# Kernel optimization log

Measured on AMD Instinct MI355X. Metric: run time of the kernel, lower is better.

## Reference

```python
import jax, jax.numpy as jnp
import numpy as np

B, S, D, DOUT = 16, 1024, 768, 256
TEMP = D ** 0.5


def setup_inputs() -> dict:
    key = jax.random.key(0)
    ks = jax.random.split(key, 16)
    emb = jax.random.normal(ks[0], (B, S, D), dtype=jnp.float32)
    mask = jax.random.randint(ks[1], (B, S), 0, 2, dtype=jnp.int32)
    scale = 0.02
    def lin(kw, kb, din, dout):
        return (jax.random.normal(kw, (din, dout), dtype=jnp.float32) * scale,
                jax.random.normal(kb, (dout,), dtype=jnp.float32) * scale)
    q_Wq, q_bq = lin(ks[2], ks[3], D, D)
    q_Wk, q_bk = lin(ks[4], ks[5], D, D)
    q_Wv, q_bv = lin(ks[6], ks[7], D, DOUT)
    d_Wq, d_bq = lin(ks[8], ks[9], D, D)
    d_Wk, d_bk = lin(ks[10], ks[11], D, D)
    d_Wv, d_bv = lin(ks[12], ks[13], D, DOUT)
    return {
        'emb': emb, 'mask': mask, 'is_query': 1,
        'query_Wq': q_Wq, 'query_bq': q_bq,
        'query_Wk': q_Wk, 'query_bk': q_bk,
        'query_Wv': q_Wv, 'query_bv': q_bv,
        'doc_Wq': d_Wq, 'doc_bq': d_bq,
        'doc_Wk': d_Wk, 'doc_bk': d_bk,
        'doc_Wv': d_Wv, 'doc_bv': d_bv,
    }


def reference(emb, mask, is_query,
              query_Wq, query_bq, query_Wk, query_bk, query_Wv, query_bv,
              doc_Wq, doc_bq, doc_Wk, doc_bk, doc_Wv, doc_bv):
    # is_query is a static Python int/bool selecting the projection set
    if is_query:
        Wq, bq, Wk, bk, Wv, bv = query_Wq, query_bq, query_Wk, query_bk, query_Wv, query_bv
    else:
        Wq, bq, Wk, bk, Wv, bv = doc_Wq, doc_bq, doc_Wk, doc_bk, doc_Wv, doc_bv
    q = jnp.einsum('bsd,de->bse', emb, Wq) + bq  # [B,S,D]
    k = jnp.einsum('bsd,de->bse', emb, Wk) + bk  # [B,S,D]
    v = jnp.einsum('bsd,de->bse', emb, Wv) + bv  # [B,S,DOUT]
    attn = jnp.einsum('bqd,bkd->bqk', q / TEMP, k)  # [B,S,S]
    attn = jnp.where(mask[:, None, :] == 0, jnp.float32(-1e9), attn)
    attn = jax.nn.softmax(attn, axis=-1)
    out = jnp.einsum('bqk,bkd->bqd', attn, v)  # [B,S,DOUT]
    return out, attn
```

## Files before the change

kernel.cpp:

```cpp
#include <hip/hip_runtime.h>
#include <hip/hip_bf16.h>

static constexpr float INV_TEMP = 0.03608439182435161f;

typedef __attribute__((ext_vector_type(8))) short bf16x8;
typedef __attribute__((ext_vector_type(4))) float f32x4;
typedef __attribute__((ext_vector_type(8))) unsigned short u16x8;
typedef __attribute__((ext_vector_type(4))) unsigned short u16x4;

__device__ __forceinline__ unsigned short f2bf(float f) {
  unsigned u = __float_as_uint(f);
  u += 0x7fffu + ((u >> 16) & 1u);
  return (unsigned short)(u >> 16);
}

__device__ __forceinline__ void async_copy16(const void* g, void* lds) {
  __builtin_amdgcn_global_load_lds(
      (const __attribute__((address_space(1))) unsigned int*)g,
      (__attribute__((address_space(3))) unsigned int*)lds, 16, 0, 0);
}

__global__ __launch_bounds__(256) void pack_emb(const float* __restrict__ src,
                                                unsigned short* __restrict__ dst) {
  long i = ((long)blockIdx.x * 256 + threadIdx.x) * 8;
  float4 a = *(const float4*)(src + i);
  float4 b = *(const float4*)(src + i + 4);
  u16x8 v;
  v[0] = f2bf(a.x); v[1] = f2bf(a.y); v[2] = f2bf(a.z); v[3] = f2bf(a.w);
  v[4] = f2bf(b.x); v[5] = f2bf(b.y); v[6] = f2bf(b.z); v[7] = f2bf(b.w);
  *(u16x8*)(dst + i) = v;
}

__global__ __launch_bounds__(256) void pack_w(
    const int* __restrict__ isq_p,
    const float* qWq, const float* qbq, const float* qWk, const float* qbk,
    const float* qWv, const float* qbv,
    const float* dWq, const float* dbq, const float* dWk, const float* dbk,
    const float* dWv, const float* dbv,
    unsigned short* __restrict__ WT, float* __restrict__ bias) {
  const int n = blockIdx.x;
  const int isq = *isq_p;
  const float* W; const float* bsrc; int col, srcN;
  if (n < 768)       { W = isq ? qWq : dWq; bsrc = isq ? qbq : dbq; col = n;        srcN = 768; }
  else if (n < 1536) { W = isq ? qWk : dWk; bsrc = isq ? qbk : dbk; col = n - 768;  srcN = 768; }
  else               { W = isq ? qWv : dWv; bsrc = isq ? qbv : dbv; col = n - 1536; srcN = 256; }
#pragma unroll
  for (int i = 0; i < 3; ++i) {
    int d = threadIdx.x + i * 256;
    WT[(long)n * 768 + d] = f2bf(W[(long)d * srcN + col]);
  }
  if (threadIdx.x == 0) bias[n] = bsrc[col];
}

template <int MODE>
__global__ __launch_bounds__(512, 2) void gemm256(
    const unsigned short* __restrict__ A, long lda, long strideA,
    const unsigned short* __restrict__ BT, long ldb, long strideB,
    void* __restrict__ Cv, long ldc, long strideC,
    const float* __restrict__ bias, float scale, int K) {
  extern __shared__ unsigned short smem[];
  const int tid = threadIdx.x;
  const int wid = tid >> 6, lane = tid & 63;
  const int wr = wid >> 2, wc = wid & 3;
  const int fr = lane & 15, fq = lane >> 4;
  const int bz = blockIdx.z;
  const unsigned short* Apan = A + (long)bz * strideA + (long)blockIdx.x * 256 * lda;
  const unsigned short* Bpan = BT + (long)bz * strideB + (long)blockIdx.y * 256 * ldb;
  const int nk = K >> 6;

  auto stage = [&](int tile, int mat, int ks, int buf) {
    const unsigned short* g = (mat ? Bpan : Apan) + (long)tile * 64 + ks * 32;
    const long ld = mat ? ldb : lda;
    unsigned short* d = smem + (((buf << 2) | (mat << 1) | ks) << 13);
#pragma unroll
    for (int i = 0; i < 2; ++i) {
      const int e = (tid + i * 512) * 8;
      const int row = e >> 5;
      const int sl = (e >> 3) & 3;
      const int ss = sl ^ ((row >> 1) & 3);
      async_copy16(g + (long)row * ld + ss * 8, d + e);
    }
  };

  const int fro = fr * 32 + ((fq ^ ((fr >> 1) & 3)) << 3);
  const int awo = fro + (wr * 128) * 32;
  const int bwo = fro + (wc * 64) * 32;

  bf16x8 a[8];
  f32x4 acc[8][4];
#pragma unroll
  for (int m = 0; m < 8; ++m)
#pragma unroll
    for (int n = 0; n < 4; ++n) acc[m][n] = f32x4{0.f, 0.f, 0.f, 0.f};

  stage(0, 0, 0, 0); stage(0, 1, 0, 0); stage(0, 0, 1, 0); stage(0, 1, 1, 0);
  if (nk > 1) {
    stage(1, 0, 0, 1); stage(1, 1, 0, 1); stage(1, 0, 1, 1);
    asm volatile("s_waitcnt vmcnt(6)" ::: "memory");
  } else {
    asm volatile("s_waitcnt vmcnt(0)" ::: "memory");
  }
  __builtin_amdgcn_sched_barrier(0);
  __builtin_amdgcn_s_barrier();

  for (int t = 0; t < nk; ++t) {
    const int p = t & 1;
    const unsigned short* A0 = smem + (((p << 2) | 0) << 13);
    const unsigned short* A1 = smem + (((p << 2) | 1) << 13);
    const unsigned short* B0 = smem + (((p << 2) | 2) << 13);
    const unsigned short* B1 = smem + (((p << 2) | 3) << 13);

    {
#pragma unroll
      for (int m = 0; m < 8; ++m) a[m] = *(const bf16x8*)(A0 + awo + m * 512);
      bf16x8 b0 = *(const bf16x8*)(B0 + bwo + 0 * 512);
      bf16x8 b1 = *(const bf16x8*)(B0 + bwo + 1 * 512);
      if (t + 1 < nk) stage(t + 1, 1, 1, (t + 1) & 1);
      __builtin_amdgcn_s_barrier();
      asm volatile("s_waitcnt lgkmcnt(0)");
      __builtin_amdgcn_sched_barrier(0);
      __builtin_amdgcn_s_setprio(1);
#pragma unroll
      for (int m = 0; m < 8; ++m) {
        acc[m][0] = __builtin_amdgcn_mfma_f32_16x16x32_bf16(a[m], b0, acc[m][0], 0, 0, 0);
        acc[m][1] = __builtin_amdgcn_mfma_f32_16x16x32_bf16(a[m], b1, acc[m][1], 0, 0, 0);
      }
      __builtin_amdgcn_s_setprio(0);
      __builtin_amdgcn_sched_barrier(0);
      __builtin_amdgcn_s_barrier();
    }
    {
      bf16x8 b2 = *(const bf16x8*)(B0 + bwo + 2 * 512);
      bf16x8 b3 = *(const bf16x8*)(B0 + bwo + 3 * 512);
      if (t + 2 < nk) stage(t + 2, 0, 0, p);
      __builtin_amdgcn_s_barrier();
      asm volatile("s_waitcnt lgkmcnt(0)");
      __builtin_amdgcn_sched_barrier(0);
      __builtin_amdgcn_s_setprio(1);
#pragma unroll
      for (int m = 0; m < 8; ++m) {
        acc[m][2] = __builtin_amdgcn_mfma_f32_16x16x32_bf16(a[m], b2, acc[m][2], 0, 0, 0);
        acc[m][3] = __builtin_amdgcn_mfma_f32_16x16x32_bf16(a[m], b3, acc[m][3], 0, 0, 0);
      }
      __builtin_amdgcn_s_setprio(0);
      __builtin_amdgcn_sched_barrier(0);
      __builtin_amdgcn_s_barrier();
    }
    {
#pragma unroll
      for (int m = 0; m < 8; ++m) a[m] = *(const bf16x8*)(A1 + awo + m * 512);
      bf16x8 b0 = *(const bf16x8*)(B1 + bwo + 0 * 512);
      bf16x8 b1 = *(const bf16x8*)(B1 + bwo + 1 * 512);
      if (t + 2 < nk) stage(t + 2, 1, 0, p);
      __builtin_amdgcn_s_barrier();
      asm volatile("s_waitcnt lgkmcnt(0)");
      __builtin_amdgcn_sched_barrier(0);
      __builtin_amdgcn_s_setprio(1);
#pragma unroll
      for (int m = 0; m < 8; ++m) {
        acc[m][0] = __builtin_amdgcn_mfma_f32_16x16x32_bf16(a[m], b0, acc[m][0], 0, 0, 0);
        acc[m][1] = __builtin_amdgcn_mfma_f32_16x16x32_bf16(a[m], b1, acc[m][1], 0, 0, 0);
      }
      __builtin_amdgcn_s_setprio(0);
      __builtin_amdgcn_sched_barrier(0);
      __builtin_amdgcn_s_barrier();
    }
    {
      bf16x8 b2 = *(const bf16x8*)(B1 + bwo + 2 * 512);
      bf16x8 b3 = *(const bf16x8*)(B1 + bwo + 3 * 512);
      if (t + 2 < nk) stage(t + 2, 0, 1, p);
      __builtin_amdgcn_s_barrier();
      asm volatile("s_waitcnt lgkmcnt(0)");
      __builtin_amdgcn_sched_barrier(0);
      __builtin_amdgcn_s_setprio(1);
#pragma unroll
      for (int m = 0; m < 8; ++m) {
        acc[m][2] = __builtin_amdgcn_mfma_f32_16x16x32_bf16(a[m], b2, acc[m][2], 0, 0, 0);
        acc[m][3] = __builtin_amdgcn_mfma_f32_16x16x32_bf16(a[m], b3, acc[m][3], 0, 0, 0);
      }
      __builtin_amdgcn_s_setprio(0);
      if (t < nk - 2) {
        asm volatile("s_waitcnt vmcnt(6)" ::: "memory");
      } else if (t == nk - 2) {
        asm volatile("s_waitcnt vmcnt(0)" ::: "memory");
      }
      __builtin_amdgcn_sched_barrier(0);
      __builtin_amdgcn_s_barrier();
    }
  }

  const long m0 = (long)blockIdx.x * 256 + wr * 128;
  const long n0 = (long)blockIdx.y * 256 + wc * 64;
#pragma unroll
  for (int m = 0; m < 8; ++m) {
#pragma unroll
    for (int n = 0; n < 4; ++n) {
      const long mm = m0 + m * 16 + fq * 4;
      const long nn = n0 + n * 16 + fr;
      f32x4 v = acc[m][n];
      if (MODE == 0) {
        unsigned short* C = (unsigned short*)Cv + (long)bz * strideC;
        const float bb = bias[nn];
#pragma unroll
        for (int r = 0; r < 4; ++r) C[(mm + r) * ldc + nn] = f2bf(v[r] + bb);
      } else {
        float* C = (float*)Cv + (long)bz * strideC;
#pragma unroll
        for (int r = 0; r < 4; ++r) C[(mm + r) * ldc + nn] = v[r] * scale;
      }
    }
  }
}

template <int MODE>
__global__ __launch_bounds__(256) void gemm_bt(
    const unsigned short* __restrict__ A, long lda, long strideA,
    const unsigned short* __restrict__ BT, long ldb, long strideB,
    void* __restrict__ Cv, long ldc, long strideC,
    const float* __restrict__ bias, float scale, int K) {
  __shared__ unsigned short Ab[2][128 * 32];
  __shared__ unsigned short Bb[2][128 * 32];
  const int tid = threadIdx.x, wid = tid >> 6, lane = tid & 63;
  const int bz = blockIdx.z;
  A  += (long)bz * strideA + (long)blockIdx.x * 128 * lda;
  BT += (long)bz * strideB + (long)blockIdx.y * 128 * ldb;
  const int srow = lane >> 2;
  const int skk  = (lane & 3) * 8;

  auto stage = [&](int buf, int kt) {
    const unsigned short* As = A + (long)kt * 32;
    const unsigned short* Bs = BT + (long)kt * 32;
#pragma unroll
    for (int i = 0; i < 2; ++i) {
      int c = wid * 2 + i;
      async_copy16(As + (long)(c * 16 + srow) * lda + skk, &Ab[buf][c * 512]);
      async_copy16(Bs + (long)(c * 16 + srow) * ldb + skk, &Bb[buf][c * 512]);
    }
  };

  f32x4 acc[4][4] = {};
  const int nk = K / 32;
  stage(0, 0);
  __syncthreads();
  int buf = 0;
  const int wr = wid >> 1, wc = wid & 1;
  const int fr = lane & 15, fq = lane >> 4;
  for (int kt = 0; kt < nk; ++kt) {
    if (kt + 1 < nk) stage(buf ^ 1, kt + 1);
    const unsigned short* Ap = &Ab[buf][(wr * 64 + fr) * 32 + fq * 8];
    const unsigned short* Bp = &Bb[buf][(wc * 64 + fr) * 32 + fq * 8];
    bf16x8 af[4], bfv[4];
#pragma unroll
    for (int mi = 0; mi < 4; ++mi) af[mi] = *(const bf16x8*)(Ap + mi * 16 * 32);
#pragma unroll
    for (int ni = 0; ni < 4; ++ni) bfv[ni] = *(const bf16x8*)(Bp + ni * 16 * 32);
#pragma unroll
    for (int mi = 0; mi < 4; ++mi)
#pragma unroll
      for (int ni = 0; ni < 4; ++ni)
        acc[mi][ni] = __builtin_amdgcn_mfma_f32_16x16x32_bf16(af[mi], bfv[ni], acc[mi][ni], 0, 0, 0);
    __syncthreads();
    buf ^= 1;
  }

  const long m0 = (long)blockIdx.x * 128 + wr * 64;
  const long n0 = (long)blockIdx.y * 128 + wc * 64;
#pragma unroll
  for (int mi = 0; mi < 4; ++mi) {
#pragma unroll
    for (int ni = 0; ni < 4; ++ni) {
      const long m = m0 + mi * 16 + fq * 4;
      const long n = n0 + ni * 16 + fr;
      f32x4 v = acc[mi][ni];
      if (MODE == 1) {
        unsigned short* C = (unsigned short*)Cv + (long)bz * strideC;
#pragma unroll
        for (int r = 0; r < 4; ++r) C[(m + r) * ldc + n] = f2bf(v[r] + bias[m + r]);
      } else {
        float* C = (float*)Cv + (long)bz * strideC;
#pragma unroll
        for (int r = 0; r < 4; ++r) C[(m + r) * ldc + n] = v[r] * scale;
      }
    }
  }
}

__global__ __launch_bounds__(256) void softmax_rows(float* __restrict__ attn,
                                                    const int* __restrict__ mask,
                                                    unsigned short* __restrict__ attn_bf) {
  const int row = blockIdx.x;
  const int b = row >> 10;
  float* p = attn + (long)row * 1024;
  const int tid = threadIdx.x, lane = tid & 63, wid = tid >> 6;
  float4 v = ((const float4*)p)[tid];
  int4 mk = ((const int4*)(mask + b * 1024))[tid];
  v.x = mk.x ? v.x : -1e9f;
  v.y = mk.y ? v.y : -1e9f;
  v.z = mk.z ? v.z : -1e9f;
  v.w = mk.w ? v.w : -1e9f;
  float mx = fmaxf(fmaxf(v.x, v.y), fmaxf(v.z, v.w));
#pragma unroll
  for (int off = 32; off; off >>= 1) mx = fmaxf(mx, __shfl_xor(mx, off));
  __shared__ float red[4];
  if (lane == 0) red[wid] = mx;
  __syncthreads();
  mx = fmaxf(fmaxf(red[0], red[1]), fmaxf(red[2], red[3]));
  float e0 = __expf(v.x - mx), e1 = __expf(v.y - mx);
  float e2 = __expf(v.z - mx), e3 = __expf(v.w - mx);
  float s = e0 + e1 + e2 + e3;
#pragma unroll
  for (int off = 32; off; off >>= 1) s += __shfl_xor(s, off);
  __shared__ float red2[4];
  if (lane == 0) red2[wid] = s;
  __syncthreads();
  s = red2[0] + red2[1] + red2[2] + red2[3];
  const float inv = 1.0f / s;
  float4 o;
  o.x = e0 * inv; o.y = e1 * inv; o.z = e2 * inv; o.w = e3 * inv;
  ((float4*)p)[tid] = o;
  u16x4 ob;
  ob[0] = f2bf(o.x); ob[1] = f2bf(o.y); ob[2] = f2bf(o.z); ob[3] = f2bf(o.w);
  *(u16x4*)(attn_bf + (long)row * 1024 + tid * 4) = ob;
}

extern "C" void kernel_launch(void* const* d_in, const int* in_sizes, int n_in,
                              void* d_out, int out_size, void* d_ws, size_t ws_size,
                              hipStream_t stream) {
  const float* emb = (const float*)d_in[0];
  const int* mask = (const int*)d_in[1];
  const int* isq = (const int*)d_in[2];
  const float* qWq = (const float*)d_in[3];  const float* qbq = (const float*)d_in[4];
  const float* qWk = (const float*)d_in[5];  const float* qbk = (const float*)d_in[6];
  const float* qWv = (const float*)d_in[7];  const float* qbv = (const float*)d_in[8];
  const float* dWq = (const float*)d_in[9];  const float* dbq = (const float*)d_in[10];
  const float* dWk = (const float*)d_in[11]; const float* dbk = (const float*)d_in[12];
  const float* dWv = (const float*)d_in[13]; const float* dbv = (const float*)d_in[14];

  char* ws = (char*)d_ws;
  unsigned short* emb_bf = (unsigned short*)ws;  ws += (size_t)16384 * 768 * 2;
  unsigned short* WT     = (unsigned short*)ws;  ws += (size_t)1792 * 768 * 2;
  float*          bias   = (float*)ws;           ws += (size_t)1792 * 4;
  unsigned short* QK     = (unsigned short*)ws;  ws += (size_t)16384 * 1536 * 2;
  unsigned short* VT     = (unsigned short*)ws;  ws += (size_t)256 * 16384 * 2;
  unsigned short* attnbf = (unsigned short*)ws;  ws += (size_t)16 * 1024 * 1024 * 2;

  float* out = (float*)d_out;
  float* attn = out + (size_t)16 * 1024 * 256;

  (void)hipFuncSetAttribute((const void*)&gemm256<0>,
                            hipFuncAttributeMaxDynamicSharedMemorySize, 131072);
  (void)hipFuncSetAttribute((const void*)&gemm256<2>,
                            hipFuncAttributeMaxDynamicSharedMemorySize, 131072);

  hipLaunchKernelGGL(pack_emb, dim3(6144), dim3(256), 0, stream, emb, emb_bf);
  hipLaunchKernelGGL(pack_w, dim3(1792), dim3(256), 0, stream, isq,
                     qWq, qbq, qWk, qbk, qWv, qbv, dWq, dbq, dWk, dbk, dWv, dbv, WT, bias);
  hipLaunchKernelGGL((gemm256<0>), dim3(64, 6, 1), dim3(512), 131072, stream,
                     emb_bf, 768L, 0L, WT, 768L, 0L, (void*)QK, 1536L, 0L, bias, 1.0f, 768);
  hipLaunchKernelGGL((gemm_bt<1>), dim3(2, 128, 1), dim3(256), 0, stream,
                     WT + (size_t)1536 * 768, 768L, 0L, emb_bf, 768L, 0L,
                     (void*)VT, 16384L, 0L, bias + 1536, 1.0f, 768);
  hipLaunchKernelGGL((gemm256<2>), dim3(4, 4, 16), dim3(512), 131072, stream,
                     QK, 1536L, (long)1024 * 1536, QK + 768, 1536L, (long)1024 * 1536,
                     (void*)attn, 1024L, (long)1024 * 1024, nullptr, INV_TEMP, 768);
  hipLaunchKernelGGL(softmax_rows, dim3(16384), dim3(256), 0, stream, attn, mask, attnbf);
  hipLaunchKernelGGL((gemm_bt<2>), dim3(8, 2, 16), dim3(256), 0, stream,
                     attnbf, 1024L, (long)1024 * 1024, VT, 16384L, 1024L,
                     (void*)out, 256L, (long)1024 * 256, nullptr, 1.0f, 1024);
}
```

Measured before the change: 183.3 us.

## Merge QK and V projections into one launch, restage k-loop, retile PV GEMM

Merges the QK projection GEMM and the transposed V projection GEMM into a single 448-block launch that shares a common 256x256 k-loop. This removes one launch and lets the small V GEMM run alongside the big one. The k-loop now splits its four quarter-phases along M (4x4 MFMA blocks) instead of along N, and the prefetch order and vmcnt waits change to match. The PV GEMM is retiled from 128x128 to 128x64 output tiles, doubling its grid to 512 blocks for better occupancy at the cost of more reloads of the A operand.

```diff
diff --git a/kernel.cpp b/kernel.cpp
--- a/kernel.cpp
+++ b/kernel.cpp
@@ -52,21 +52,14 @@
   if (threadIdx.x == 0) bias[n] = bsrc[col];
 }
 
-template <int MODE>
-__global__ __launch_bounds__(512, 2) void gemm256(
-    const unsigned short* __restrict__ A, long lda, long strideA,
-    const unsigned short* __restrict__ BT, long ldb, long strideB,
-    void* __restrict__ Cv, long ldc, long strideC,
-    const float* __restrict__ bias, float scale, int K) {
-  extern __shared__ unsigned short smem[];
+__device__ __forceinline__ void k_loop_256(
+    const unsigned short* __restrict__ Apan, long lda,
+    const unsigned short* __restrict__ Bpan, long ldb,
+    int nk, unsigned short* smem, f32x4 (&acc)[8][4]) {
   const int tid = threadIdx.x;
   const int wid = tid >> 6, lane = tid & 63;
   const int wr = wid >> 2, wc = wid & 3;
   const int fr = lane & 15, fq = lane >> 4;
-  const int bz = blockIdx.z;
-  const unsigned short* Apan = A + (long)bz * strideA + (long)blockIdx.x * 256 * lda;
-  const unsigned short* Bpan = BT + (long)bz * strideB + (long)blockIdx.y * 256 * ldb;
-  const int nk = K >> 6;
 
   auto stage = [&](int tile, int mat, int ks, int buf) {
     const unsigned short* g = (mat ? Bpan : Apan) + (long)tile * 64 + ks * 32;
@@ -86,17 +79,10 @@
   const int awo = fro + (wr * 128) * 32;
   const int bwo = fro + (wc * 64) * 32;
 
-  bf16x8 a[8];
-  f32x4 acc[8][4];
-#pragma unroll
-  for (int m = 0; m < 8; ++m)
-#pragma unroll
-    for (int n = 0; n < 4; ++n) acc[m][n] = f32x4{0.f, 0.f, 0.f, 0.f};
-
   stage(0, 0, 0, 0); stage(0, 1, 0, 0); stage(0, 0, 1, 0); stage(0, 1, 1, 0);
   if (nk > 1) {
-    stage(1, 0, 0, 1); stage(1, 1, 0, 1); stage(1, 0, 1, 1);
-    asm volatile("s_waitcnt vmcnt(6)" ::: "memory");
+    stage(1, 0, 0, 1); stage(1, 1, 1, 1);
+    asm volatile("s_waitcnt vmcnt(4)" ::: "memory");
   } else {
     asm volatile("s_waitcnt vmcnt(0)" ::: "memory");
   }
@@ -109,123 +95,182 @@
     const unsigned short* A1 = smem + (((p << 2) | 1) << 13);
     const unsigned short* B0 = smem + (((p << 2) | 2) << 13);
     const unsigned short* B1 = smem + (((p << 2) | 3) << 13);
-
-    {
-#pragma unroll
-      for (int m = 0; m < 8; ++m) a[m] = *(const bf16x8*)(A0 + awo + m * 512);
-      bf16x8 b0 = *(const bf16x8*)(B0 + bwo + 0 * 512);
-      bf16x8 b1 = *(const bf16x8*)(B0 + bwo + 1 * 512);
-      if (t + 1 < nk) stage(t + 1, 1, 1, (t + 1) & 1);
-      __builtin_amdgcn_s_barrier();
-      asm volatile("s_waitcnt lgkmcnt(0)");
-      __builtin_amdgcn_sched_barrier(0);
-      __builtin_amdgcn_s_setprio(1);
-#pragma unroll
-      for (int m = 0; m < 8; ++m) {
-        acc[m][0] = __builtin_amdgcn_mfma_f32_16x16x32_bf16(a[m], b0, acc[m][0], 0, 0, 0);
-        acc[m][1] = __builtin_amdgcn_mfma_f32_16x16x32_bf16(a[m], b1, acc[m][1], 0, 0, 0);
+    bf16x8 a[4], b[4];
+
+#pragma unroll
+    for (int m = 0; m < 4; ++m) a[m] = *(const bf16x8*)(A0 + awo + m * 512);
+#pragma unroll
+    for (int n = 0; n < 4; ++n) b[n] = *(const bf16x8*)(B0 + bwo + n * 512);
+    if (t + 1 < nk) stage(t + 1, 0, 1, (t + 1) & 1);
+    __builtin_amdgcn_s_barrier();
+    asm volatile("s_waitcnt lgkmcnt(0)");
+    __builtin_amdgcn_sched_barrier(0);
+    __builtin_amdgcn_s_setprio(1);
+#pragma unroll
+    for (int m = 0; m < 4; ++m)
+#pragma unroll
+      for (int n = 0; n < 4; ++n)
+        acc[m][n] = __builtin_amdgcn_mfma_f32_16x16x32_bf16(a[m], b[n], acc[m][n], 0, 0, 0);
+    __builtin_amdgcn_s_setprio(0);
+    __builtin_amdgcn_sched_barrier(0);
+    __builtin_amdgcn_s_barrier();
+
+#pragma unroll
+    for (int m = 0; m < 4; ++m) a[m] = *(const bf16x8*)(A0 + awo + (4 + m) * 512);
+    if (t + 1 < nk) stage(t + 1, 1, 0, (t + 1) & 1);
+    __builtin_amdgcn_s_barrier();
+    asm volatile("s_waitcnt lgkmcnt(0)");
+    __builtin_amdgcn_sched_barrier(0);
+    __builtin_amdgcn_s_setprio(1);
+#pragma unroll
+    for (int m = 0; m < 4; ++m)
+#pragma unroll
+      for (int n = 0; n < 4; ++n)
+        acc[4 + m][n] = __builtin_amdgcn_mfma_f32_16x16x32_bf16(a[m], b[n], acc[4 + m][n], 0, 0, 0);
+    __builtin_amdgcn_s_setprio(0);
+    __builtin_amdgcn_sched_barrier(0);
+    __builtin_amdgcn_s_barrier();
+
+#pragma unroll
+    for (int m = 0; m < 4; ++m) a[m] = *(const bf16x8*)(A1 + awo + m * 512);
+#pragma unroll
+    for (int n = 0; n < 4; ++n) b[n] = *(const bf16x8*)(B1 + bwo + n * 512);
+    if (t + 2 < nk) stage(t + 2, 0, 0, p);
+    __builtin_amdgcn_s_barrier();
+    asm volatile("s_waitcnt lgkmcnt(0)");
+    __builtin_amdgcn_sched_barrier(0);
+    __builtin_amdgcn_s_setprio(1);
+#pragma unroll
+    for (int m = 0; m < 4; ++m)
+#pragma unroll
+      for (int n = 0; n < 4; ++n)
+        acc[m][n] = __builtin_amdgcn_mfma_f32_16x16x32_bf16(a[m], b[n], acc[m][n], 0, 0, 0);
+    __builtin_amdgcn_s_setprio(0);
+    __builtin_amdgcn_sched_barrier(0);
+    __builtin_amdgcn_s_barrier();
+
+#pragma unroll
+    for (int m = 0; m < 4; ++m) a[m] = *(const bf16x8*)(A1 + awo + (4 + m) * 512);
+    if (t + 2 < nk) stage(t + 2, 1, 1, p);
+    __builtin_amdgcn_s_barrier();
+    asm volatile("s_waitcnt lgkmcnt(0)");
+    __builtin_amdgcn_sched_barrier(0);
+    __builtin_amdgcn_s_setprio(1);
+#pragma unroll
+    for (int m = 0; m < 4; ++m)
+#pragma unroll
+      for (int n = 0; n < 4; ++n)
+        acc[4 + m][n] = __builtin_amdgcn_mfma_f32_16x16x32_bf16(a[m], b[n], acc[4 + m][n], 0, 0, 0);
+    __builtin_amdgcn_s_setprio(0);
+    if (t < nk - 2) {
+      asm volatile("s_waitcnt vmcnt(4)" ::: "memory");
+    } else if (t == nk - 2) {
+      asm volatile("s_waitcnt vmcnt(0)" ::: "memory");
+    }
+    __builtin_amdgcn_sched_barrier(0);
+    __builtin_amdgcn_s_barrier();
+  }
+}
+
+__global__ __launch_bounds__(512, 2) void proj256(
+    const unsigned short* __restrict__ emb_bf,
+    const unsigned short* __restrict__ WT,
+    const float* __restrict__ bias,
+    unsigned short* __restrict__ QK,
+    unsigned short* __restrict__ VT) {
+  extern __shared__ unsigned short smem[];
+  const int id = blockIdx.x;
+  const unsigned short* Apan;
+  const unsigned short* Bpan;
+  if (id < 384) {
+    Apan = emb_bf + (long)(id & 63) * 256 * 768;
+    Bpan = WT + (long)(id >> 6) * 256 * 768;
+  } else {
+    Apan = WT + (long)1536 * 768;
+    Bpan = emb_bf + (long)(id - 384) * 256 * 768;
+  }
+  f32x4 acc[8][4];
+#pragma unroll
+  for (int m = 0; m < 8; ++m)
+#pragma unroll
+    for (int n = 0; n < 4; ++n) acc[m][n] = f32x4{0.f, 0.f, 0.f, 0.f};
+
+  k_loop_256(Apan, 768, Bpan, 768, 12, smem, acc);
+
+  const int wid = threadIdx.x >> 6, lane = threadIdx.x & 63;
+  const int wr = wid >> 2, wc = wid & 3;
+  const int fr = lane & 15, fq = lane >> 4;
+  if (id < 384) {
+    const long x = id & 63, y = id >> 6;
+#pragma unroll
+    for (int m = 0; m < 8; ++m)
+#pragma unroll
+      for (int n = 0; n < 4; ++n) {
+        const long mm = x * 256 + wr * 128 + m * 16 + fq * 4;
+        const long nn = y * 256 + wc * 64 + n * 16 + fr;
+        const float bb = bias[nn];
+        f32x4 v = acc[m][n];
+#pragma unroll
+        for (int r = 0; r < 4; ++r) QK[(mm + r) * 1536 + nn] = f2bf(v[r] + bb);
       }
-      __builtin_amdgcn_s_setprio(0);
-      __builtin_amdgcn_sched_barrier(0);
-      __builtin_amdgcn_s_barrier();
+  } else {
+    const long v0 = id - 384;
+#pragma unroll
+    for (int m = 0; m < 8; ++m)
+#pragma unroll
+      for (int n = 0; n < 4; ++n) {
+        const long mm = wr * 128 + m * 16 + fq * 4;
+        const long nn = v0 * 256 + wc * 64 + n * 16 + fr;
+        f32x4 v = acc[m][n];
+#pragma unroll
+        for (int r = 0; r < 4; ++r)
+          VT[(mm + r) * 16384 + nn] = f2bf(v[r] + bias[1536 + mm + r]);
+      }
+  }
+}
+
+__global__ __launch_bounds__(512, 2) void logits256(
+    const unsigned short* __restrict__ QK, float* __restrict__ attn) {
+  extern __shared__ unsigned short smem[];
+  const int bz = blockIdx.z;
+  const unsigned short* Apan = QK + (long)bz * 1024 * 1536 + (long)blockIdx.x * 256 * 1536;
+  const unsigned short* Bpan = QK + 768 + (long)bz * 1024 * 1536 + (long)blockIdx.y * 256 * 1536;
+  f32x4 acc[8][4];
+#pragma unroll
+  for (int m = 0; m < 8; ++m)
+#pragma unroll
+    for (int n = 0; n < 4; ++n) acc[m][n] = f32x4{0.f, 0.f, 0.f, 0.f};
+
+  k_loop_256(Apan, 1536, Bpan, 1536, 12, smem, acc);
+
+  const int wid = threadIdx.x >> 6, lane = threadIdx.x & 63;
+  const int wr = wid >> 2, wc = wid & 3;
+  const int fr = lane & 15, fq = lane >> 4;
+  float* C = attn + (long)bz * 1024 * 1024;
+#pragma unroll
+  for (int m = 0; m < 8; ++m)
+#pragma unroll
+    for (int n = 0; n < 4; ++n) {
+      const long mm = (long)blockIdx.x * 256 + wr * 128 + m * 16 + fq * 4;
+      const long nn = (long)blockIdx.y * 256 + wc * 64 + n * 16 + fr;
+      f32x4 v = acc[m][n];
+#pragma unroll
+      for (int r = 0; r < 4; ++r) C[(mm + r) * 1024 + nn] = v[r] * INV_TEMP;
     }
-    {
-      bf16x8 b2 = *(const bf16x8*)(B0 + bwo + 2 * 512);
-      bf16x8 b3 = *(const bf16x8*)(B0 + bwo + 3 * 512);
-      if (t + 2 < nk) stage(t + 2, 0, 0, p);
-      __builtin_amdgcn_s_barrier();
-      asm volatile("s_waitcnt lgkmcnt(0)");
-      __builtin_amdgcn_sched_barrier(0);
-      __builtin_amdgcn_s_setprio(1);
-#pragma unroll
-      for (int m = 0; m < 8; ++m) {
-        acc[m][2] = __builtin_amdgcn_mfma_f32_16x16x32_bf16(a[m], b2, acc[m][2], 0, 0, 0);
-        acc[m][3] = __builtin_amdgcn_mfma_f32_16x16x32_bf16(a[m], b3, acc[m][3], 0, 0, 0);
-      }
-      __builtin_amdgcn_s_setprio(0);
-      __builtin_amdgcn_sched_barrier(0);
-      __builtin_amdgcn_s_barrier();
-    }
-    {
-#pragma unroll
-      for (int m = 0; m < 8; ++m) a[m] = *(const bf16x8*)(A1 + awo + m * 512);
-      bf16x8 b0 = *(const bf16x8*)(B1 + bwo + 0 * 512);
-      bf16x8 b1 = *(const bf16x8*)(B1 + bwo + 1 * 512);
-      if (t + 2 < nk) stage(t + 2, 1, 0, p);
-      __builtin_amdgcn_s_barrier();
-      asm volatile("s_waitcnt lgkmcnt(0)");
-      __builtin_amdgcn_sched_barrier(0);
-      __builtin_amdgcn_s_setprio(1);
-#pragma unroll
-      for (int m = 0; m < 8; ++m) {
-        acc[m][0] = __builtin_amdgcn_mfma_f32_16x16x32_bf16(a[m], b0, acc[m][0], 0, 0, 0);
-        acc[m][1] = __builtin_amdgcn_mfma_f32_16x16x32_bf16(a[m], b1, acc[m][1], 0, 0, 0);
-      }
-      __builtin_amdgcn_s_setprio(0);
-      __builtin_amdgcn_sched_barrier(0);
-      __builtin_amdgcn_s_barrier();
-    }
-    {
-      bf16x8 b2 = *(const bf16x8*)(B1 + bwo + 2 * 512);
-      bf16x8 b3 = *(const bf16x8*)(B1 + bwo + 3 * 512);
-      if (t + 2 < nk) stage(t + 2, 0, 1, p);
-      __builtin_amdgcn_s_barrier();
-      asm volatile("s_waitcnt lgkmcnt(0)");
-      __builtin_amdgcn_sched_barrier(0);
-      __builtin_amdgcn_s_setprio(1);
-#pragma unroll
-      for (int m = 0; m < 8; ++m) {
-        acc[m][2] = __builtin_amdgcn_mfma_f32_16x16x32_bf16(a[m], b2, acc[m][2], 0, 0, 0);
-        acc[m][3] = __builtin_amdgcn_mfma_f32_16x16x32_bf16(a[m], b3, acc[m][3], 0, 0, 0);
-      }
-      __builtin_amdgcn_s_setprio(0);
-      if (t < nk - 2) {
-        asm volatile("s_waitcnt vmcnt(6)" ::: "memory");
-      } else if (t == nk - 2) {
-        asm volatile("s_waitcnt vmcnt(0)" ::: "memory");
-      }
-      __builtin_amdgcn_sched_barrier(0);
-      __builtin_amdgcn_s_barrier();
-    }
-  }
-
-  const long m0 = (long)blockIdx.x * 256 + wr * 128;
-  const long n0 = (long)blockIdx.y * 256 + wc * 64;
-#pragma unroll
-  for (int m = 0; m < 8; ++m) {
-#pragma unroll
-    for (int n = 0; n < 4; ++n) {
-      const long mm = m0 + m * 16 + fq * 4;
-      const long nn = n0 + n * 16 + fr;
-      f32x4 v = acc[m][n];
-      if (MODE == 0) {
-        unsigned short* C = (unsigned short*)Cv + (long)bz * strideC;
-        const float bb = bias[nn];
-#pragma unroll
-        for (int r = 0; r < 4; ++r) C[(mm + r) * ldc + nn] = f2bf(v[r] + bb);
-      } else {
-        float* C = (float*)Cv + (long)bz * strideC;
-#pragma unroll
-        for (int r = 0; r < 4; ++r) C[(mm + r) * ldc + nn] = v[r] * scale;
-      }
-    }
-  }
-}
-
-template <int MODE>
-__global__ __launch_bounds__(256) void gemm_bt(
-    const unsigned short* __restrict__ A, long lda, long strideA,
-    const unsigned short* __restrict__ BT, long ldb, long strideB,
-    void* __restrict__ Cv, long ldc, long strideC,
-    const float* __restrict__ bias, float scale, int K) {
+}
+
+__global__ __launch_bounds__(256) void gemm_pv(
+    const unsigned short* __restrict__ attnbf,
+    const unsigned short* __restrict__ VT,
+    float* __restrict__ out) {
   __shared__ unsigned short Ab[2][128 * 32];
-  __shared__ unsigned short Bb[2][128 * 32];
+  __shared__ unsigned short Bb[2][64 * 32];
   const int tid = threadIdx.x, wid = tid >> 6, lane = tid & 63;
   const int bz = blockIdx.z;
-  A  += (long)bz * strideA + (long)blockIdx.x * 128 * lda;
-  BT += (long)bz * strideB + (long)blockIdx.y * 128 * ldb;
+  const unsigned short* A = attnbf + (long)bz * 1024 * 1024 + (long)blockIdx.x * 128 * 1024;
+  const unsigned short* BT = VT + (long)bz * 1024 + (long)blockIdx.y * 64 * 16384;
   const int srow = lane >> 2;
-  const int skk  = (lane & 3) * 8;
+  const int skk = (lane & 3) * 8;
 
   auto stage = [&](int buf, int kt) {
     const unsigned short* As = A + (long)kt * 32;
@@ -233,13 +278,13 @@
 #pragma unroll
     for (int i = 0; i < 2; ++i) {
       int c = wid * 2 + i;
-      async_copy16(As + (long)(c * 16 + srow) * lda + skk, &Ab[buf][c * 512]);
-      async_copy16(Bs + (long)(c * 16 + srow) * ldb + skk, &Bb[buf][c * 512]);
+      async_copy16(As + (long)(c * 16 + srow) * 1024 + skk, &Ab[buf][c * 512]);
     }
+    async_copy16(Bs + (long)(wid * 16 + srow) * 16384 + skk, &Bb[buf][wid * 512]);
   };
 
-  f32x4 acc[4][4] = {};
-  const int nk = K / 32;
+  f32x4 acc[4][2] = {};
+  const int nk = 32;
   stage(0, 0);
   __syncthreads();
   int buf = 0;
@@ -248,41 +293,34 @@
   for (int kt = 0; kt < nk; ++kt) {
     if (kt + 1 < nk) stage(buf ^ 1, kt + 1);
     const unsigned short* Ap = &Ab[buf][(wr * 64 + fr) * 32 + fq * 8];
-    const unsigned short* Bp = &Bb[buf][(wc * 64 + fr) * 32 + fq * 8];
-    bf16x8 af[4], bfv[4];
+    const unsigned short* Bp = &Bb[buf][(wc * 32 + fr) * 32 + fq * 8];
+    bf16x8 af[4], bfv[2];
 #pragma unroll
     for (int mi = 0; mi < 4; ++mi) af[mi] = *(const bf16x8*)(Ap + mi * 16 * 32);
 #pragma unroll
-    for (int ni = 0; ni < 4; ++ni) bfv[ni] = *(const bf16x8*)(Bp + ni * 16 * 32);
+    for (int ni = 0; ni < 2; ++ni) bfv[ni] = *(const bf16x8*)(Bp + ni * 16 * 32);
 #pragma unroll
     for (int mi = 0; mi < 4; ++mi)
 #pragma unroll
-      for (int ni = 0; ni < 4; ++ni)
+      for (int ni = 0; ni < 2; ++ni)
         acc[mi][ni] = __builtin_amdgcn_mfma_f32_16x16x32_bf16(af[mi], bfv[ni], acc[mi][ni], 0, 0, 0);
     __syncthreads();
     buf ^= 1;
   }
 
+  float* C = out + (long)bz * 1024 * 256;
   const long m0 = (long)blockIdx.x * 128 + wr * 64;
-  const long n0 = (long)blockIdx.y * 128 + wc * 64;
-#pragma unroll
-  for (int mi = 0; mi < 4; ++mi) {
-#pragma unroll
-    for (int ni = 0; ni < 4; ++ni) {
+  const long n0 = (long)blockIdx.y * 64 + wc * 32;
+#pragma unroll
+  for (int mi = 0; mi < 4; ++mi)
+#pragma unroll
+    for (int ni = 0; ni < 2; ++ni) {
       const long m = m0 + mi * 16 + fq * 4;
       const long n = n0 + ni * 16 + fr;
       f32x4 v = acc[mi][ni];
-      if (MODE == 1) {
-        unsigned short* C = (unsigned short*)Cv + (long)bz * strideC;
-#pragma unroll
-        for (int r = 0; r < 4; ++r) C[(m + r) * ldc + n] = f2bf(v[r] + bias[m + r]);
-      } else {
-        float* C = (float*)Cv + (long)bz * strideC;
-#pragma unroll
-        for (int r = 0; r < 4; ++r) C[(m + r) * ldc + n] = v[r] * scale;
-      }
+#pragma unroll
+      for (int r = 0; r < 4; ++r) C[(m + r) * 256 + n] = v[r];
     }
-  }
 }
 
 __global__ __launch_bounds__(256) void softmax_rows(float* __restrict__ attn,
@@ -347,24 +385,17 @@
   float* out = (float*)d_out;
   float* attn = out + (size_t)16 * 1024 * 256;
 
-  (void)hipFuncSetAttribute((const void*)&gemm256<0>,
+  (void)hipFuncSetAttribute((const void*)&proj256,
                             hipFuncAttributeMaxDynamicSharedMemorySize, 131072);
-  (void)hipFuncSetAttribute((const void*)&gemm256<2>,
+  (void)hipFuncSetAttribute((const void*)&logits256,
                             hipFuncAttributeMaxDynamicSharedMemorySize, 131072);
 
   hipLaunchKernelGGL(pack_emb, dim3(6144), dim3(256), 0, stream, emb, emb_bf);
   hipLaunchKernelGGL(pack_w, dim3(1792), dim3(256), 0, stream, isq,
                      qWq, qbq, qWk, qbk, qWv, qbv, dWq, dbq, dWk, dbk, dWv, dbv, WT, bias);
-  hipLaunchKernelGGL((gemm256<0>), dim3(64, 6, 1), dim3(512), 131072, stream,
-                     emb_bf, 768L, 0L, WT, 768L, 0L, (void*)QK, 1536L, 0L, bias, 1.0f, 768);
-  hipLaunchKernelGGL((gemm_bt<1>), dim3(2, 128, 1), dim3(256), 0, stream,
-                     WT + (size_t)1536 * 768, 768L, 0L, emb_bf, 768L, 0L,
-                     (void*)VT, 16384L, 0L, bias + 1536, 1.0f, 768);
-  hipLaunchKernelGGL((gemm256<2>), dim3(4, 4, 16), dim3(512), 131072, stream,
-                     QK, 1536L, (long)1024 * 1536, QK + 768, 1536L, (long)1024 * 1536,
-                     (void*)attn, 1024L, (long)1024 * 1024, nullptr, INV_TEMP, 768);
+  hipLaunchKernelGGL(proj256, dim3(448), dim3(512), 131072, stream,
+                     emb_bf, WT, bias, QK, VT);
+  hipLaunchKernelGGL(logits256, dim3(4, 4, 16), dim3(512), 131072, stream, QK, attn);
   hipLaunchKernelGGL(softmax_rows, dim3(16384), dim3(256), 0, stream, attn, mask, attnbf);
-  hipLaunchKernelGGL((gemm_bt<2>), dim3(8, 2, 16), dim3(256), 0, stream,
-                     attnbf, 1024L, (long)1024 * 1024, VT, 16384L, 1024L,
-                     (void*)out, 256L, (long)1024 * 256, nullptr, 1.0f, 1024);
-}
+  hipLaunchKernelGGL(gemm_pv, dim3(8, 4, 16), dim3(256), 0, stream, attnbf, VT, out);
+}
```

Result: faster. 163.3 us (-10.9%).
